# Performance work log

Measured on AMD Instinct MI355X. Metric: run time of the kernel, lower is better.

Reference implementation:

```python
import jax, jax.numpy as jnp
import numpy as np

SCALE_H = 160.0
SCALE_W = 160.0
ALIGNED = False


def setup_inputs() -> dict:
    key = jax.random.key(0)
    k1, k2, k3, k4 = jax.random.split(key, 4)
    N, C, H, W, K = 8, 256, 160, 160, 1024
    feat = jax.random.normal(k1, (N, C, H, W), dtype=jnp.float32)
    b = jax.random.randint(k2, (K,), 0, N).astype(jnp.float32)
    xs = jnp.sort(jax.random.uniform(k3, (K, 2), dtype=jnp.float32), axis=1)
    ys = jnp.sort(jax.random.uniform(k4, (K, 2), dtype=jnp.float32), axis=1)
    rois = jnp.stack([b, xs[:, 0], ys[:, 0], xs[:, 1], ys[:, 1]], axis=1)
    return {"input_feature_map": feat, "rois": rois,
            "output_height": 14, "output_width": 14}


def _roi_align(feat, rois, output_height, output_width):
    N, C, H, W = feat.shape
    K = rois.shape[0]
    b = rois[:, 0].astype(jnp.int32)
    x1 = rois[:, 1] * SCALE_W
    y1 = rois[:, 2] * SCALE_H
    x2 = rois[:, 3] * SCALE_W
    y2 = rois[:, 4] * SCALE_H
    # normalized [0,1] grid over the ROI interior
    gx = jnp.linspace(0.0, 1.0, output_width, dtype=feat.dtype)
    gy = jnp.linspace(0.0, 1.0, output_height, dtype=feat.dtype)
    fx = x1[:, None, None] + gx[None, None, :] * (x2 - x1)[:, None, None]  # (K,1,Wo)
    fy = y1[:, None, None] + gy[None, :, None] * (y2 - y1)[:, None, None]  # (K,Ho,1)
    # convert to grid_sample normalized coords, then back to pixel coords
    if ALIGNED:
        ngx = fx / (W - 1) * 2 - 1
        ngy = fy / (H - 1) * 2 - 1
        ix = (ngx + 1) * 0.5 * (W - 1)
        iy = (ngy + 1) * 0.5 * (H - 1)
    else:
        ngx = fx / W * 2 - 1
        ngy = fy / H * 2 - 1
        ix = ((ngx + 1) * W - 1) * 0.5
        iy = ((ngy + 1) * H - 1) * 0.5
    x0 = jnp.floor(ix).astype(jnp.int32)
    y0 = jnp.floor(iy).astype(jnp.int32)
    x1i = x0 + 1
    y1i = y0 + 1
    wx1 = ix - x0.astype(feat.dtype)
    wx0 = 1.0 - wx1
    wy1 = iy - y0.astype(feat.dtype)
    wy0 = 1.0 - wy1
    # zeros padding: out-of-bounds corners contribute 0
    vx0 = ((x0 >= 0) & (x0 < W)).astype(feat.dtype)
    vx1 = ((x1i >= 0) & (x1i < W)).astype(feat.dtype)
    vy0 = ((y0 >= 0) & (y0 < H)).astype(feat.dtype)
    vy1 = ((y1i >= 0) & (y1i < H)).astype(feat.dtype)
    x0c = jnp.clip(x0, 0, W - 1)
    x1c = jnp.clip(x1i, 0, W - 1)
    y0c = jnp.clip(y0, 0, H - 1)
    y1c = jnp.clip(y1i, 0, H - 1)
    # flat gather table: (N*H*W, C) -- no per-ROI feature-map duplication
    featf = jnp.transpose(feat, (0, 2, 3, 1)).reshape(N * H * W, C)
    bb = b[:, None, None]  # (K,1,1)

    def corner(yy, xx, w):
        lin = (bb * H + yy) * W + xx  # broadcast -> (K,Ho,Wo)
        lin = jnp.broadcast_to(lin, (K, output_height, output_width))
        v = featf[lin.reshape(-1)].reshape(K, output_height, output_width, C)
        w = jnp.broadcast_to(w, (K, output_height, output_width))
        return v * w[..., None]

    out = (corner(y0c, x0c, wy0 * wx0 * vy0 * vx0)
           + corner(y0c, x1c, wy0 * wx1 * vy0 * vx1)
           + corner(y1c, x0c, wy1 * wx0 * vy1 * vx0)
           + corner(y1c, x1c, wy1 * wx1 * vy1 * vx1))
    return jnp.transpose(out, (0, 3, 1, 2))  # (K, C, Ho, Wo)


def reference(input_feature_map, rois, output_height, output_width):
    return _roi_align(input_feature_map, rois, int(output_height), int(output_width))
```

## Files before the change

kernel.cpp:

```cpp
#include <hip/hip_runtime.h>
#include <hip/hip_fp16.h>


#define FM_N 8
#define FM_C 256
#define FM_H 160
#define FM_W 160
#define PLANE (FM_H * FM_W)
#define PLANE4 (PLANE / 4)
#define OH 14
#define OW 14
#define OSP (OH * OW)
#define KMAX 1024
#define SCALE_HW 160.0f
#define MAIN_BLK 1024
#define NCP 2
#define STG_IT 7

typedef float f4 __attribute__((ext_vector_type(4)));

#define WS_KLIST_OFF 16
#define WS_SAMPLES_BYTE_OFF 4224

__global__ void setup_kernel(const float* __restrict__ rois, int K,
                             int* __restrict__ ws) {
  __shared__ int cnt[FM_N];
  __shared__ int koff[FM_N];
  const int t = threadIdx.x;
  if (t < FM_N) cnt[t] = 0;
  __syncthreads();
  int myb = -1, pos = 0;
  if (t < K) {
    myb = (int)rois[t * 5];
    pos = atomicAdd(&cnt[myb], 1);
  }
  __syncthreads();
  if (t == 0) {
    int acc = 0;
    for (int b = 0; b < FM_N; ++b) { koff[b] = acc; acc += cnt[b]; }
  }
  __syncthreads();
  if (t < K) ws[WS_KLIST_OFF + koff[myb] + pos] = t;
  if (t < FM_N) { ws[t] = cnt[t]; ws[FM_N + t] = koff[t]; }
}

__global__ __launch_bounds__(256) void precompute_kernel(
    const float* __restrict__ rois, const int* __restrict__ ws, int K,
    uint2* __restrict__ samples) {
  const int g = blockIdx.x * 256 + threadIdx.x;
  if (g >= K * OSP) return;
  const int slot = g / OSP;
  const int s = g - slot * OSP;
  const int k = ws[WS_KLIST_OFF + slot];

  const float x1 = rois[k * 5 + 1] * SCALE_HW;
  const float y1 = rois[k * 5 + 2] * SCALE_HW;
  const float x2 = rois[k * 5 + 3] * SCALE_HW;
  const float y2 = rois[k * 5 + 4] * SCALE_HW;

  const int oy = s / OW;
  const int ox = s - oy * OW;
  const float gx = (float)ox * (1.0f / (OW - 1));
  const float gy = (float)oy * (1.0f / (OH - 1));

  const float ix = x1 + gx * (x2 - x1) - 0.5f;
  const float iy = y1 + gy * (y2 - y1) - 0.5f;

  const float fx0 = floorf(ix);
  const float fy0 = floorf(iy);
  const int x0 = (int)fx0;
  const int y0 = (int)fy0;
  const float wx1 = ix - fx0;
  const float wy1 = iy - fy0;

  const float vx0 = (x0 >= 0 && x0 < FM_W) ? 1.0f : 0.0f;
  const float vx1 = (x0 + 1 >= 0 && x0 + 1 < FM_W) ? 1.0f : 0.0f;
  const unsigned vy0 = (y0 >= 0 && y0 < FM_H) ? 1u : 0u;
  const unsigned vy1 = (y0 + 1 >= 0 && y0 + 1 < FM_H) ? 1u : 0u;

  const int x0c = min(max(x0, 0), FM_W - 1);
  const int x1c = min(max(x0 + 1, 0), FM_W - 1);
  const int y0c = min(max(y0, 0), FM_H - 1);
  const int y1c = min(max(y0 + 1, 0), FM_H - 1);

  const unsigned o00 = (unsigned)(y0c * FM_W + x0c);
  const unsigned dx = (unsigned)(x1c - x0c);
  const unsigned dyr = (unsigned)(y1c - y0c);
  unsigned wq = (unsigned)(wy1 * 8192.0f + 0.5f);
  wq = wq > 8191u ? 8191u : wq;

  const __half2 axh = __floats2half2_rn((1.0f - wx1) * vx0, wx1 * vx1);

  uint2 sd;
  sd.x = o00 | (dx << 15) | (dyr << 16) | (wq << 17) | (vy0 << 30) | (vy1 << 31);
  sd.y = *(const unsigned*)&axh;
  samples[(size_t)slot * OSP + s] = sd;
}

__global__ __launch_bounds__(MAIN_BLK) void roi_align_main_kernel(
    const float* __restrict__ feat, const int* __restrict__ ws,
    const uint2* __restrict__ samples, float* __restrict__ out) {
  __shared__ __align__(16) __half2 plane[PLANE];
  __shared__ int klist[KMAX];

  const int b = blockIdx.y;
  const int p0 = blockIdx.x * NCP;
  const int t = threadIdx.x;

  const int cnt = ws[b];
  const int koff = ws[FM_N + b];
  for (int i = t; i < cnt; i += MAIN_BLK)
    klist[i] = ws[WS_KLIST_OFF + koff + i];

  const uint2* __restrict__ sam = samples + (size_t)koff * OSP;
  const int total = cnt * OSP;
  const f4* __restrict__ fbase =
      (const f4*)feat + (size_t)b * FM_C * PLANE4;

  f4 ra[STG_IT], rb[STG_IT];

  auto load_pair = [&](int p) {
    const f4* __restrict__ srcA = fbase + (size_t)(2 * p) * PLANE4;
    const f4* __restrict__ srcB = srcA + PLANE4;
#pragma unroll
    for (int i = 0; i < STG_IT; ++i) {
      const int idx = t + i * MAIN_BLK;
      if (idx < PLANE4) {
        ra[i] = __builtin_nontemporal_load(&srcA[idx]);
        rb[i] = __builtin_nontemporal_load(&srcB[idx]);
      }
    }
  };

  auto write_plane = [&]() {
    uint4* __restrict__ pl4 = (uint4*)plane;
#pragma unroll
    for (int i = 0; i < STG_IT; ++i) {
      const int idx = t + i * MAIN_BLK;
      if (idx < PLANE4) {
        const __half2 h0 = __floats2half2_rn(ra[i].x, rb[i].x);
        const __half2 h1 = __floats2half2_rn(ra[i].y, rb[i].y);
        const __half2 h2 = __floats2half2_rn(ra[i].z, rb[i].z);
        const __half2 h3 = __floats2half2_rn(ra[i].w, rb[i].w);
        uint4 u;
        u.x = *(const unsigned*)&h0;
        u.y = *(const unsigned*)&h1;
        u.z = *(const unsigned*)&h2;
        u.w = *(const unsigned*)&h3;
        pl4[idx] = u;
      }
    }
  };

  auto compute_pair = [&](int c0) {
#pragma unroll 2
    for (int w = t; w < total; w += MAIN_BLK) {
      const uint2 sd = sam[w];
      const unsigned kl = (unsigned)w / OSP;
      const int s = w - (int)kl * OSP;
      const int k = klist[kl];

      const int o00 = (int)(sd.x & 0x7FFFu);
      const int dx = (int)((sd.x >> 15) & 1u);
      const int o10 = o00 + (int)((sd.x >> 16) & 1u) * FM_W;

      const __half2 p00 = plane[o00];
      const __half2 p01 = plane[o00 + dx];
      const __half2 p10 = plane[o10];
      const __half2 p11 = plane[o10 + dx];

      const float wy1 = (float)((sd.x >> 17) & 0x1FFFu) * (1.0f / 8192.0f);
      const float ay0 = ((sd.x >> 30) & 1u) ? (1.0f - wy1) : 0.0f;
      const float ay1 = (sd.x >> 31) ? wy1 : 0.0f;
      const __half2 ax = *(const __half2*)&sd.y;
      const float ax0 = __low2float(ax), ax1 = __high2float(ax);

      const float vA = ay0 * (ax0 * __low2float(p00) + ax1 * __low2float(p01)) +
                       ay1 * (ax0 * __low2float(p10) + ax1 * __low2float(p11));
      const float vB = ay0 * (ax0 * __high2float(p00) + ax1 * __high2float(p01)) +
                       ay1 * (ax0 * __high2float(p10) + ax1 * __high2float(p11));

      const size_t ob = ((size_t)k * FM_C + c0) * OSP + s;
      out[ob] = vA;
      out[ob + OSP] = vB;
    }
  };

  load_pair(p0);
  write_plane();
  __syncthreads();

  for (int cp = 0; cp < NCP; ++cp) {
    if (cp + 1 < NCP) load_pair(p0 + cp + 1);
    compute_pair(2 * (p0 + cp));
    if (cp + 1 < NCP) {
      __syncthreads();
      write_plane();
      __syncthreads();
    }
  }
}

extern "C" void kernel_launch(void* const* d_in, const int* in_sizes, int n_in,
                              void* d_out, int out_size, void* d_ws, size_t ws_size,
                              hipStream_t stream) {
  const float* feat = (const float*)d_in[0];
  const float* rois = (const float*)d_in[1];
  float* out = (float*)d_out;
  int* ws = (int*)d_ws;
  uint2* samples = (uint2*)((char*)d_ws + WS_SAMPLES_BYTE_OFF);

  const int K = in_sizes[1] / 5;

  setup_kernel<<<1, 1024, 0, stream>>>(rois, K, ws);
  precompute_kernel<<<(K * OSP + 255) / 256, 256, 0, stream>>>(rois, ws, K,
                                                               samples);
  roi_align_main_kernel<<<dim3(FM_C / 2 / NCP, FM_N), MAIN_BLK, 0, stream>>>(
      feat, ws, samples, out);
}
```

Measured before the change: 100.7 us.

## Pack horizontal bilinear taps into half2 FMA with padded shared plane

Horizontal interpolation now runs as packed half2 multiply-add on adjacent plane entries. A padded shared buffer plus a shifted base index let both x taps read as consecutive entries without the dx branch. klist is prescaled to output base offsets so the per-sample address math is simpler, and the unroll factor rises from 2 to 4. The half-precision horizontal blend lowers accuracy slightly, and the new index encoding changes the bit layout of the samples.

```diff
diff --git a/kernel.cpp b/kernel.cpp
--- a/kernel.cpp
+++ b/kernel.cpp
@@ -73,8 +73,8 @@
   const float wx1 = ix - fx0;
   const float wy1 = iy - fy0;
 
-  const float vx0 = (x0 >= 0 && x0 < FM_W) ? 1.0f : 0.0f;
-  const float vx1 = (x0 + 1 >= 0 && x0 + 1 < FM_W) ? 1.0f : 0.0f;
+  const bool vx0 = (x0 >= 0 && x0 < FM_W);
+  const bool vx1 = (x0 + 1 >= 0 && x0 + 1 < FM_W);
   const unsigned vy0 = (y0 >= 0 && y0 < FM_H) ? 1u : 0u;
   const unsigned vy1 = (y0 + 1 >= 0 && y0 + 1 < FM_H) ? 1u : 0u;
 
@@ -83,16 +83,19 @@
   const int y0c = min(max(y0, 0), FM_H - 1);
   const int y1c = min(max(y0 + 1, 0), FM_H - 1);
 
-  const unsigned o00 = (unsigned)(y0c * FM_W + x0c);
-  const unsigned dx = (unsigned)(x1c - x0c);
+  const int o00 = y0c * FM_W + x0c;
+  const int o01 = y0c * FM_W + x1c;
+  const int bx = vx1 ? (o01 - 1) : o00;
+  const unsigned bxs = (unsigned)(bx + 4);
   const unsigned dyr = (unsigned)(y1c - y0c);
   unsigned wq = (unsigned)(wy1 * 8192.0f + 0.5f);
   wq = wq > 8191u ? 8191u : wq;
 
-  const __half2 axh = __floats2half2_rn((1.0f - wx1) * vx0, wx1 * vx1);
+  const __half2 axh = __floats2half2_rn((1.0f - wx1) * (vx0 ? 1.0f : 0.0f),
+                                        wx1 * (vx1 ? 1.0f : 0.0f));
 
   uint2 sd;
-  sd.x = o00 | (dx << 15) | (dyr << 16) | (wq << 17) | (vy0 << 30) | (vy1 << 31);
+  sd.x = bxs | (dyr << 15) | (wq << 16) | (vy0 << 29) | (vy1 << 30);
   sd.y = *(const unsigned*)&axh;
   samples[(size_t)slot * OSP + s] = sd;
 }
@@ -100,7 +103,7 @@
 __global__ __launch_bounds__(MAIN_BLK) void roi_align_main_kernel(
     const float* __restrict__ feat, const int* __restrict__ ws,
     const uint2* __restrict__ samples, float* __restrict__ out) {
-  __shared__ __align__(16) __half2 plane[PLANE];
+  __shared__ __align__(16) __half2 planeBuf[PLANE + 8];
   __shared__ int klist[KMAX];
 
   const int b = blockIdx.y;
@@ -110,12 +113,16 @@
   const int cnt = ws[b];
   const int koff = ws[FM_N + b];
   for (int i = t; i < cnt; i += MAIN_BLK)
-    klist[i] = ws[WS_KLIST_OFF + koff + i];
+    klist[i] = ws[WS_KLIST_OFF + koff + i] * (FM_C * OSP);
+  if (t < 4) {
+    planeBuf[t] = __floats2half2_rn(0.0f, 0.0f);
+    planeBuf[PLANE + 4 + t] = __floats2half2_rn(0.0f, 0.0f);
+  }
 
   const uint2* __restrict__ sam = samples + (size_t)koff * OSP;
   const int total = cnt * OSP;
-  const f4* __restrict__ fbase =
-      (const f4*)feat + (size_t)b * FM_C * PLANE4;
+  const f4* __restrict__ fbase = (const f4*)feat + (size_t)b * FM_C * PLANE4;
+  __half2* __restrict__ planeP = planeBuf + 4;
 
   f4 ra[STG_IT], rb[STG_IT];
 
@@ -133,7 +140,7 @@
   };
 
   auto write_plane = [&]() {
-    uint4* __restrict__ pl4 = (uint4*)plane;
+    uint4* __restrict__ pl4 = (uint4*)planeP;
 #pragma unroll
     for (int i = 0; i < STG_IT; ++i) {
       const int idx = t + i * MAIN_BLK;
@@ -153,36 +160,38 @@
   };
 
   auto compute_pair = [&](int c0) {
-#pragma unroll 2
+    float* __restrict__ outc = out + (size_t)c0 * OSP;
+#pragma unroll 4
     for (int w = t; w < total; w += MAIN_BLK) {
       const uint2 sd = sam[w];
       const unsigned kl = (unsigned)w / OSP;
       const int s = w - (int)kl * OSP;
-      const int k = klist[kl];
-
-      const int o00 = (int)(sd.x & 0x7FFFu);
-      const int dx = (int)((sd.x >> 15) & 1u);
-      const int o10 = o00 + (int)((sd.x >> 16) & 1u) * FM_W;
-
-      const __half2 p00 = plane[o00];
-      const __half2 p01 = plane[o00 + dx];
-      const __half2 p10 = plane[o10];
-      const __half2 p11 = plane[o10 + dx];
-
-      const float wy1 = (float)((sd.x >> 17) & 0x1FFFu) * (1.0f / 8192.0f);
-      const float ay0 = ((sd.x >> 30) & 1u) ? (1.0f - wy1) : 0.0f;
-      const float ay1 = (sd.x >> 31) ? wy1 : 0.0f;
+      const int kbase = klist[kl];
+
+      const int bxs = (int)(sd.x & 0x7FFFu);
+      const int b2 = bxs + (int)((sd.x >> 15) & 1u) * FM_W;
+
+      const __half2 pL0 = planeP[bxs - 4];
+      const __half2 pR0 = planeP[bxs - 3];
+      const __half2 pL1 = planeP[b2 - 4];
+      const __half2 pR1 = planeP[b2 - 3];
+
       const __half2 ax = *(const __half2*)&sd.y;
-      const float ax0 = __low2float(ax), ax1 = __high2float(ax);
-
-      const float vA = ay0 * (ax0 * __low2float(p00) + ax1 * __low2float(p01)) +
-                       ay1 * (ax0 * __low2float(p10) + ax1 * __low2float(p11));
-      const float vB = ay0 * (ax0 * __high2float(p00) + ax1 * __high2float(p01)) +
-                       ay1 * (ax0 * __high2float(p10) + ax1 * __high2float(p11));
-
-      const size_t ob = ((size_t)k * FM_C + c0) * OSP + s;
-      out[ob] = vA;
-      out[ob + OSP] = vB;
+      const __half2 axl = __half2half2(__low2half(ax));
+      const __half2 axr = __half2half2(__high2half(ax));
+      const __half2 hx0 = __hfma2(pR0, axr, __hmul2(pL0, axl));
+      const __half2 hx1 = __hfma2(pR1, axr, __hmul2(pL1, axl));
+
+      const float wy1 = (float)((sd.x >> 16) & 0x1FFFu) * (1.0f / 8192.0f);
+      const float ay0 = ((sd.x >> 29) & 1u) ? (1.0f - wy1) : 0.0f;
+      const float ay1 = ((sd.x >> 30) & 1u) ? wy1 : 0.0f;
+
+      const float vA = ay0 * __low2float(hx0) + ay1 * __low2float(hx1);
+      const float vB = ay0 * __high2float(hx0) + ay1 * __high2float(hx1);
+
+      const size_t ob = (size_t)(kbase + s);
+      outc[ob] = vA;
+      outc[ob + OSP] = vB;
     }
   };
 
```

Measured after the change: 98.74 us. No clear change (-2.0%).
